# Kernel tuning notes

Measured on AMD Instinct MI355X. Metric: run time of the kernel, lower is better.

Reference implementation:

```python
import jax, jax.numpy as jnp
import numpy as np

B, H, W, C = 16, 64, 64, 256
WS = 8          # window_size
SHIFT = 4       # shift_size
HEADS = 8
HEAD_DIM = C // HEADS
N = WS * WS     # tokens per window
HID = 4 * C     # mlp hidden
EPS = 1e-5


def _rel_pos_index():
    coords = np.stack(np.meshgrid(np.arange(WS), np.arange(WS), indexing='ij'))  # [2,WS,WS]
    flat = coords.reshape(2, -1)                                                  # [2,N]
    rel = (flat[:, :, None] - flat[:, None, :]).transpose(1, 2, 0)                # [N,N,2]
    rel[:, :, 0] += WS - 1
    rel[:, :, 1] += WS - 1
    rel[:, :, 0] *= 2 * WS - 1
    return rel.sum(-1).astype(np.int32)                                           # [N,N]


def _attn_mask():
    # shifted-window region ids, identical to get_img_mask (shift == WS//2)
    img = np.zeros((H, W), dtype=np.float32)
    cnt = 0
    for hs in (slice(0, H - WS), slice(H - WS, H - SHIFT), slice(H - SHIFT, H)):
        for ws_ in (slice(0, W - WS), slice(W - WS, W - SHIFT), slice(W - SHIFT, W)):
            img[hs, ws_] = cnt
            cnt += 1
    mw = img.reshape(H // WS, WS, W // WS, WS).transpose(0, 2, 1, 3).reshape(-1, N)  # [nW,N]
    diff = mw[:, None, :] - mw[:, :, None]
    return np.where(diff != 0, -100.0, 0.0).astype(np.float32)                        # [nW,N,N]


def window_partition(x):
    # [B,H,W,C] -> [B*nW, N, C]
    x = x.reshape(B, H // WS, WS, W // WS, WS, C)
    return x.transpose(0, 1, 3, 2, 4, 5).reshape(-1, N, C)


def window_reverse(w):
    # [B*nW, WS, WS, C] -> [B,H,W,C]
    x = w.reshape(B, H // WS, W // WS, WS, WS, C)
    return x.transpose(0, 1, 3, 2, 4, 5).reshape(B, H, W, C)


def layernorm(x, g, b):
    mu = jnp.mean(x, -1, keepdims=True)
    var = jnp.mean(jnp.square(x - mu), -1, keepdims=True)
    return (x - mu) * jax.lax.rsqrt(var + EPS) * g + b


def setup_inputs() -> dict:
    key = jax.random.key(0)
    ks = jax.random.split(key, 12)
    s = 0.02
    return {
        'x': jax.random.normal(ks[0], (B, H, W, C), jnp.float32),
        'ln1_g': jnp.ones((C,), jnp.float32),
        'ln1_b': jnp.zeros((C,), jnp.float32),
        'qkv_w': jax.random.normal(ks[1], (C, 3 * C), jnp.float32) * s,
        'qkv_b': jnp.zeros((3 * C,), jnp.float32),
        'proj_w': jax.random.normal(ks[2], (C, C), jnp.float32) * s,
        'proj_b': jnp.zeros((C,), jnp.float32),
        'rel_bias_table': jax.random.normal(ks[3], ((2 * WS - 1) ** 2, HEADS), jnp.float32) * s,
        'ln2_g': jnp.ones((C,), jnp.float32),
        'ln2_b': jnp.zeros((C,), jnp.float32),
        'mlp_w1': jax.random.normal(ks[4], (C, HID), jnp.float32) * s,
        'mlp_b1': jnp.zeros((HID,), jnp.float32),
        'mlp_w2': jax.random.normal(ks[5], (HID, C), jnp.float32) * s,
        'mlp_b2': jnp.zeros((C,), jnp.float32),
        'rel_index': jnp.asarray(_rel_pos_index()),  # [N,N] int32, constant
    }


def reference(x, ln1_g, ln1_b, qkv_w, qkv_b, proj_w, proj_b, rel_bias_table,
              ln2_g, ln2_b, mlp_w1, mlp_b1, mlp_w2, mlp_b2, rel_index):
    attn_mask = jnp.asarray(_attn_mask())                 # [nW,N,N]
    nW = attn_mask.shape[0]

    shortcut = x.reshape(B, H * W, C)
    h = layernorm(shortcut, ln1_g, ln1_b).reshape(B, H, W, C)

    # cyclic shift + window partition
    h = jnp.roll(h, shift=(-SHIFT, -SHIFT), axis=(1, 2))
    xw = window_partition(h)                              # [B*nW, N, C]

    # window attention with relative position bias
    qkv = xw @ qkv_w + qkv_b                              # [B*nW, N, 3C]
    qkv = qkv.reshape(-1, N, 3, HEADS, HEAD_DIM).transpose(2, 0, 3, 1, 4)
    q, k, v = qkv[0], qkv[1], qkv[2]                      # [B*nW, heads, N, hd]
    attn = jnp.einsum('whnd,whmd->whnm', q * (HEAD_DIM ** -0.5), k)
    bias = rel_bias_table[rel_index]                      # [N,N,heads]
    attn = attn + bias.transpose(2, 0, 1)[None]           # [B*nW,heads,N,N]
    attn = attn.reshape(B, nW, HEADS, N, N) + attn_mask[None, :, None]
    attn = jax.nn.softmax(attn.reshape(-1, HEADS, N, N), axis=-1)
    out = jnp.einsum('whnm,whmd->whnd', attn, v)
    out = out.transpose(0, 2, 1, 3).reshape(-1, N, C)
    out = out @ proj_w + proj_b                           # [B*nW, N, C]

    # window reverse + reverse shift
    out = window_reverse(out.reshape(-1, WS, WS, C))
    out = jnp.roll(out, shift=(SHIFT, SHIFT), axis=(1, 2)).reshape(B, H * W, C)

    h = shortcut + out
    m = layernorm(h, ln2_g, ln2_b)
    m = jax.nn.gelu(m @ mlp_w1 + mlp_b1) @ mlp_w2 + mlp_b2
    h = h + m
    return h.reshape(B, H, W, C)
```

## Files before the change

kernel.cpp:

```cpp
#include <hip/hip_runtime.h>


typedef __attribute__((ext_vector_type(8))) short bf16x8;
typedef __attribute__((ext_vector_type(4))) float f32x4;
typedef __attribute__((ext_vector_type(16))) float f32x16;

__device__ __forceinline__ float bf2f(unsigned short h) {
    union { unsigned int u; float f; } c; c.u = ((unsigned int)h) << 16; return c.f;
}
__device__ __forceinline__ unsigned short f2bf(float f) {
    union { float f; unsigned int u; } c; c.f = f;
    unsigned int u = c.u;
    return (unsigned short)((u + 0x7FFFu + ((u >> 16) & 1u)) >> 16);
}
__device__ __forceinline__ unsigned int cvtpk_bf16(float lo, float hi) {
    unsigned int r;
    asm volatile("v_cvt_pk_bf16_f32 %0, %1, %2" : "=v"(r) : "v"(lo), "v"(hi));
    return r;
}
__device__ __forceinline__ void perm32swap(unsigned int& a, unsigned int& b) {
    asm volatile("v_permlane32_swap_b32 %0, %1" : "+v"(a), "+v"(b));
}
__device__ __forceinline__ int remap_row(int row) {
    int b  = row >> 12;
    int w6 = (row >> 6) & 63;
    int n  = row & 63;
    int hp = (((w6 >> 3) << 3) + (n >> 3) + 4) & 63;
    int wp = (((w6 & 7) << 3) + (n & 7) + 4) & 63;
    return (b << 12) | (hp << 6) | wp;
}
__device__ __forceinline__ float gelu_f(float v) {
    float u = 1.5957691216057308f * (v + 0.044715f * v * v * v);
    return v / (1.0f + __expf(-u));
}
__device__ __forceinline__ void gload16(const unsigned short* g, unsigned short* l) {
    __builtin_amdgcn_global_load_lds(
        (const __attribute__((address_space(1))) void*)g,
        (__attribute__((address_space(3))) void*)l, 16, 0, 0);
}

__global__ __launch_bounds__(256) void ln_kernel(
    const float* __restrict__ in, const float* __restrict__ g,
    const float* __restrict__ b, unsigned short* __restrict__ out, int remap)
{
    int wave = threadIdx.x >> 6, lane = threadIdx.x & 63;
    int row = (blockIdx.x << 2) + wave;
    int src = remap ? remap_row(row) : row;
    float4 xv = *(const float4*)(in + (size_t)src * 256 + (lane << 2));
    float s  = xv.x + xv.y + xv.z + xv.w;
    float ss = xv.x*xv.x + xv.y*xv.y + xv.z*xv.z + xv.w*xv.w;
#pragma unroll
    for (int off = 32; off; off >>= 1) {
        s  += __shfl_xor(s,  off, 64);
        ss += __shfl_xor(ss, off, 64);
    }
    float mu  = s * (1.0f / 256.0f);
    float inv = rsqrtf(ss * (1.0f / 256.0f) - mu * mu + 1e-5f);
    float4 gv = *(const float4*)(g + (lane << 2));
    float4 bv = *(const float4*)(b + (lane << 2));
    ushort4 o;
    o.x = f2bf((xv.x - mu) * inv * gv.x + bv.x);
    o.y = f2bf((xv.y - mu) * inv * gv.y + bv.y);
    o.z = f2bf((xv.z - mu) * inv * gv.z + bv.z);
    o.w = f2bf((xv.w - mu) * inv * gv.w + bv.w);
    *(ushort4*)(out + (size_t)row * 256 + (lane << 2)) = o;
}

__global__ __launch_bounds__(256) void bias_expand_kernel(
    const float* __restrict__ table, const int* __restrict__ relidx,
    float* __restrict__ out)
{
    int i = blockIdx.x * 256 + threadIdx.x;
    int head = i >> 12;
    int q = (i >> 6) & 63;
    int k = i & 63;
    out[i] = table[relidx[q * 64 + k] * 8 + head];
}

__global__ __launch_bounds__(256) void convert_T_kernel(
    const float* __restrict__ in, unsigned short* __restrict__ out, int K, int N)
{
    __shared__ float t[32][33];
    int kb = K >> 5;
    int bk = (blockIdx.x % kb) << 5;
    int bn = (blockIdx.x / kb) << 5;
    int r = threadIdx.x >> 5, c = threadIdx.x & 31;
#pragma unroll
    for (int i = 0; i < 4; ++i)
        t[r + i * 8][c] = in[(size_t)(bk + r + i * 8) * N + bn + c];
    __syncthreads();
#pragma unroll
    for (int i = 0; i < 4; ++i)
        out[(size_t)(bn + r + i * 8) * K + bk + c] = f2bf(t[c][r + i * 8]);
}

template<int OUT_BF16, int DO_GELU, int RESID, int QSCALE>
__global__ __launch_bounds__(256) void mgemm_kernel(
    const unsigned short* __restrict__ A, const unsigned short* __restrict__ BT,
    const float* __restrict__ bias, void* __restrict__ outp,
    const float* __restrict__ resid, int M, int N, int K)
{
    __shared__ unsigned short As[2][128 * 32];
    __shared__ unsigned short Bs[2][128 * 32];

    const int cpx = (int)gridDim.x >> 3;
    const int bid = ((int)blockIdx.x & 7) * cpx + ((int)blockIdx.x >> 3);

    const int nb = N >> 7;
    const int m0 = (bid / nb) << 7;
    const int n0 = (bid % nb) << 7;
    const int tid  = threadIdx.x;
    const int wid  = tid >> 6;
    const int lane = tid & 63;
    const int wm = (wid >> 1) << 6;
    const int wn = (wid & 1) << 6;

    const unsigned short* Ag = A  + (size_t)m0 * K;
    const unsigned short* Bg = BT + (size_t)n0 * K;
    const int s0 = tid, s1 = tid + 256;
    const size_t ra0 = (size_t)(s0 >> 2) * K + ((s0 & 3) << 3);
    const size_t ra1 = (size_t)(s1 >> 2) * K + ((s1 & 3) << 3);

    f32x4 acc[4][4] = {};
    const int fr = lane & 15;
    const int fk = (lane >> 4) << 3;

    gload16(Ag + ra0, As[0] + s0 * 8);
    gload16(Ag + ra1, As[0] + s1 * 8);
    gload16(Bg + ra0, Bs[0] + s0 * 8);
    gload16(Bg + ra1, Bs[0] + s1 * 8);
    __syncthreads();

    int cur = 0;
    for (int k0 = 0; k0 < K; k0 += 32) {
        if (k0 + 32 < K) {
            const int nxt = cur ^ 1;
            gload16(Ag + ra0 + k0 + 32, As[nxt] + s0 * 8);
            gload16(Ag + ra1 + k0 + 32, As[nxt] + s1 * 8);
            gload16(Bg + ra0 + k0 + 32, Bs[nxt] + s0 * 8);
            gload16(Bg + ra1 + k0 + 32, Bs[nxt] + s1 * 8);
        }

        bf16x8 af[4], bfr[4];
#pragma unroll
        for (int i = 0; i < 4; ++i)
            af[i] = *(const bf16x8*)(As[cur] + (wm + i * 16 + fr) * 32 + fk);
#pragma unroll
        for (int j = 0; j < 4; ++j)
            bfr[j] = *(const bf16x8*)(Bs[cur] + (wn + j * 16 + fr) * 32 + fk);
#pragma unroll
        for (int i = 0; i < 4; ++i)
#pragma unroll
            for (int j = 0; j < 4; ++j)
                acc[i][j] = __builtin_amdgcn_mfma_f32_16x16x32_bf16(
                    af[i], bfr[j], acc[i][j], 0, 0, 0);
        __syncthreads();
        cur ^= 1;
    }

#pragma unroll
    for (int i = 0; i < 4; ++i) {
#pragma unroll
        for (int j = 0; j < 4; ++j) {
            const int col = n0 + wn + j * 16 + (lane & 15);
            const float bv = bias[col];
#pragma unroll
            for (int v = 0; v < 4; ++v) {
                const int row = m0 + wm + i * 16 + ((lane >> 4) << 2) + v;
                float val = acc[i][j][v] + bv;
                if (QSCALE) { if (col < 256) val *= 0.17677669529663687f; }
                if (DO_GELU) val = gelu_f(val);
                if (OUT_BF16) {
                    ((unsigned short*)outp)[(size_t)row * N + col] = f2bf(val);
                } else {
                    const int orow = (RESID == 2) ? remap_row(row) : row;
                    const float r = RESID ? resid[(size_t)orow * N + col] : 0.0f;
                    ((float*)outp)[(size_t)orow * N + col] = r + val;
                }
            }
        }
    }
}

__global__ __launch_bounds__(64, 3) void attn_kernel(
    const unsigned short* __restrict__ qkv,
    const float* __restrict__ bexp,
    unsigned short* __restrict__ out)
{
    __shared__ unsigned short VT[2048];
    const int bid  = blockIdx.x;
    const int widx = bid & 1023;
    const int head = bid >> 10;
    const int l  = threadIdx.x;
    const int lo = l & 31, hi = l >> 5;

    const unsigned short* base = qkv + (size_t)widx * 64 * 768;

#pragma unroll
    for (int c = 0; c < 4; ++c) {
        union { bf16x8 v; unsigned short s[8]; } u;
        u.v = *(const bf16x8*)(base + (size_t)l * 768 + 512 + head * 32 + c * 8);
#pragma unroll
        for (int e = 0; e < 8; ++e) {
            int d = c * 8 + e;
            int wb = ((d * 64 + l) * 2) ^ ((d & 7) << 4);
            *(unsigned short*)((char*)VT + wb) = u.s[e];
        }
    }

    f32x16 acc[2][2] = {};
#pragma unroll
    for (int kd = 0; kd < 2; ++kd) {
        const int coff = head * 32 + kd * 16 + hi * 8;
        bf16x8 kf0 = *(const bf16x8*)(base + (size_t)lo        * 768 + 256 + coff);
        bf16x8 kf1 = *(const bf16x8*)(base + (size_t)(32 + lo) * 768 + 256 + coff);
        bf16x8 qf0 = *(const bf16x8*)(base + (size_t)lo        * 768 + coff);
        bf16x8 qf1 = *(const bf16x8*)(base + (size_t)(32 + lo) * 768 + coff);
        acc[0][0] = __builtin_amdgcn_mfma_f32_32x32x16_bf16(kf0, qf0, acc[0][0], 0, 0, 0);
        acc[0][1] = __builtin_amdgcn_mfma_f32_32x32x16_bf16(kf0, qf1, acc[0][1], 0, 0, 0);
        acc[1][0] = __builtin_amdgcn_mfma_f32_32x32x16_bf16(kf1, qf0, acc[1][0], 0, 0, 0);
        acc[1][1] = __builtin_amdgcn_mfma_f32_32x32x16_bf16(kf1, qf1, acc[1][1], 0, 0, 0);
    }

#pragma unroll
    for (int qb = 0; qb < 2; ++qb) {
        const float* bq = bexp + head * 4096 + (qb * 32 + lo) * 64;
#pragma unroll
        for (int kb = 0; kb < 2; ++kb)
#pragma unroll
            for (int j = 0; j < 4; ++j) {
                float4 b4 = *(const float4*)(bq + kb * 32 + j * 8 + hi * 4);
                acc[kb][qb][4 * j + 0] += b4.x;
                acc[kb][qb][4 * j + 1] += b4.y;
                acc[kb][qb][4 * j + 2] += b4.z;
                acc[kb][qb][4 * j + 3] += b4.w;
            }
    }

    const int w6 = widx & 63;
    if (((w6 >> 3) == 7) || ((w6 & 7) == 7)) {
#pragma unroll
        for (int qb = 0; qb < 2; ++qb) {
            int nq = qb * 32 + lo;
            int phq = ((w6 >> 3) << 3) + (nq >> 3), pwq = ((w6 & 7) << 3) + (nq & 7);
            int rq = ((phq < 56) ? 0 : ((phq < 60) ? 1 : 2)) * 3
                   + ((pwq < 56) ? 0 : ((pwq < 60) ? 1 : 2));
#pragma unroll
            for (int kb = 0; kb < 2; ++kb)
#pragma unroll
                for (int r = 0; r < 16; ++r) {
                    int nk = kb * 32 + (r & 3) + 8 * (r >> 2) + 4 * hi;
                    int phk = ((w6 >> 3) << 3) + (nk >> 3), pwk = ((w6 & 7) << 3) + (nk & 7);
                    int rk = ((phk < 56) ? 0 : ((phk < 60) ? 1 : 2)) * 3
                           + ((pwk < 56) ? 0 : ((pwk < 60) ? 1 : 2));
                    if (rk != rq) acc[kb][qb][r] -= 100.0f;
                }
        }
    }

#pragma unroll
    for (int qb = 0; qb < 2; ++qb) {
        float mx = acc[0][qb][0];
#pragma unroll
        for (int r = 1; r < 16; ++r) mx = fmaxf(mx, acc[0][qb][r]);
#pragma unroll
        for (int r = 0; r < 16; ++r) mx = fmaxf(mx, acc[1][qb][r]);
        mx = fmaxf(mx, __shfl_xor(mx, 32, 64));
        float sum = 0.f;
#pragma unroll
        for (int kb = 0; kb < 2; ++kb)
#pragma unroll
            for (int r = 0; r < 16; ++r) {
                float e = __expf(acc[kb][qb][r] - mx);
                acc[kb][qb][r] = e;
                sum += e;
            }
        sum += __shfl_xor(sum, 32, 64);
        float inv = 1.0f / sum;
#pragma unroll
        for (int kb = 0; kb < 2; ++kb)
#pragma unroll
            for (int r = 0; r < 16; ++r) acc[kb][qb][r] *= inv;
    }

    f32x16 o[2] = {};
#pragma unroll
    for (int ks = 0; ks < 4; ++ks) {
        const int s8 = (ks & 1) * 8, kb = ks >> 1;
        const int rb = ((lo * 64 + 16 * ks + 8 * hi) * 2) ^ ((lo & 7) << 4);
        bf16x8 vb = *(const bf16x8*)((const char*)VT + rb);
#pragma unroll
        for (int qb = 0; qb < 2; ++qb) {
            unsigned int a0 = cvtpk_bf16(acc[kb][qb][s8 + 0], acc[kb][qb][s8 + 1]);
            unsigned int b0 = cvtpk_bf16(acc[kb][qb][s8 + 4], acc[kb][qb][s8 + 5]);
            unsigned int a1 = cvtpk_bf16(acc[kb][qb][s8 + 2], acc[kb][qb][s8 + 3]);
            unsigned int b1 = cvtpk_bf16(acc[kb][qb][s8 + 6], acc[kb][qb][s8 + 7]);
            perm32swap(a0, b0);
            perm32swap(a1, b1);
            union { unsigned int u[4]; bf16x8 v; } w;
            w.u[0] = a0; w.u[1] = a1; w.u[2] = b0; w.u[3] = b1;
            o[qb] = __builtin_amdgcn_mfma_f32_32x32x16_bf16(w.v, vb, o[qb], 0, 0, 0);
        }
    }

    unsigned short* ob = out + (size_t)widx * 64 * 256 + head * 32 + lo;
#pragma unroll
    for (int qb = 0; qb < 2; ++qb)
#pragma unroll
        for (int r = 0; r < 16; ++r) {
            int q = qb * 32 + (r & 3) + 8 * (r >> 2) + 4 * hi;
            ob[(size_t)q * 256] = f2bf(o[qb][r]);
        }
}

extern "C" void kernel_launch(void* const* d_in, const int* in_sizes, int n_in,
                              void* d_out, int out_size, void* d_ws, size_t ws_size,
                              hipStream_t stream)
{
    const float* x      = (const float*)d_in[0];
    const float* ln1_g  = (const float*)d_in[1];
    const float* ln1_b  = (const float*)d_in[2];
    const float* qkv_w  = (const float*)d_in[3];
    const float* qkv_b  = (const float*)d_in[4];
    const float* proj_w = (const float*)d_in[5];
    const float* proj_b = (const float*)d_in[6];
    const float* table  = (const float*)d_in[7];
    const float* ln2_g  = (const float*)d_in[8];
    const float* ln2_b  = (const float*)d_in[9];
    const float* w1     = (const float*)d_in[10];
    const float* b1     = (const float*)d_in[11];
    const float* w2     = (const float*)d_in[12];
    const float* b2     = (const float*)d_in[13];
    const int*   relidx = (const int*)d_in[14];
    float* out = (float*)d_out;

    char* w = (char*)d_ws;
    unsigned short* xw   = (unsigned short*)w;
    unsigned short* qkvb = (unsigned short*)(w + (32u << 20));
    float*          h2   = (float*)(w + (160u << 20));
    float*          bexp = (float*)(w + (224u << 20));
    unsigned short* qkvT = (unsigned short*)(w + (224u << 20) + (128u << 10));
    unsigned short* prjT = qkvT + 768 * 256;
    unsigned short* w1T  = prjT + 256 * 256;
    unsigned short* w2T  = w1T + 1024 * 256;

    convert_T_kernel<<<192, 256, 0, stream>>>(qkv_w, qkvT, 256, 768);
    convert_T_kernel<<< 64, 256, 0, stream>>>(proj_w, prjT, 256, 256);
    convert_T_kernel<<<256, 256, 0, stream>>>(w1, w1T, 256, 1024);
    convert_T_kernel<<<256, 256, 0, stream>>>(w2, w2T, 1024, 256);
    ln_kernel<<<16384, 256, 0, stream>>>(x, ln1_g, ln1_b, xw, 1);
    bias_expand_kernel<<<128, 256, 0, stream>>>(table, relidx, bexp);
    mgemm_kernel<1, 0, 0, 1><<<512 * 6, 256, 0, stream>>>(xw, qkvT, qkv_b, (void*)qkvb,
                                                          nullptr, 65536, 768, 256);
    attn_kernel<<<8192, 64, 0, stream>>>(qkvb, bexp, xw);
    mgemm_kernel<0, 0, 2, 0><<<512 * 2, 256, 0, stream>>>(xw, prjT, proj_b, (void*)h2,
                                                          x, 65536, 256, 256);
    ln_kernel<<<16384, 256, 0, stream>>>(h2, ln2_g, ln2_b, xw, 0);
    mgemm_kernel<1, 1, 0, 0><<<512 * 8, 256, 0, stream>>>(xw, w1T, b1, (void*)qkvb,
                                                          nullptr, 65536, 1024, 256);
    mgemm_kernel<0, 0, 1, 0><<<512 * 2, 256, 0, stream>>>(qkvb, w2T, b2, (void*)out,
                                                          h2, 65536, 256, 1024);
}
```

Before: 323.5 us.

## Fuse MLP fc1+GELU+fc2 into one kernel and swizzle GEMM LDS layout

Replaces the two MLP GEMM launches with a single fused kernel. Each block keeps a 64-row activation tile in LDS, computes 128-column hidden chunks with GELU into LDS, and accumulates the second GEMM in registers, so the 65536x1024 bf16 hidden tensor never goes to HBM. The generic GEMM also gets an XOR swizzle on its LDS tiles to cut bank conflicts. In exchange, the fused kernel runs only 1024 blocks with heavy LDS use (about 80KB), which lowers occupancy and adds many barriers per chunk.

```diff
diff --git a/kernel.cpp b/kernel.cpp
--- a/kernel.cpp
+++ b/kernel.cpp
@@ -118,12 +118,13 @@
     const unsigned short* Ag = A  + (size_t)m0 * K;
     const unsigned short* Bg = BT + (size_t)n0 * K;
     const int s0 = tid, s1 = tid + 256;
-    const size_t ra0 = (size_t)(s0 >> 2) * K + ((s0 & 3) << 3);
-    const size_t ra1 = (size_t)(s1 >> 2) * K + ((s1 & 3) << 3);
+    const size_t ra0 = (size_t)(s0 >> 2) * K + (((s0 & 3) ^ ((s0 >> 2) & 3)) << 3);
+    const size_t ra1 = (size_t)(s1 >> 2) * K + (((s1 & 3) ^ ((s1 >> 2) & 3)) << 3);
 
     f32x4 acc[4][4] = {};
     const int fr = lane & 15;
-    const int fk = (lane >> 4) << 3;
+    const int fq = lane >> 4;
+    const int axor = ((fq ^ (fr & 3)) << 3);
 
     gload16(Ag + ra0, As[0] + s0 * 8);
     gload16(Ag + ra1, As[0] + s1 * 8);
@@ -144,10 +145,10 @@
         bf16x8 af[4], bfr[4];
 #pragma unroll
         for (int i = 0; i < 4; ++i)
-            af[i] = *(const bf16x8*)(As[cur] + (wm + i * 16 + fr) * 32 + fk);
+            af[i] = *(const bf16x8*)(As[cur] + (wm + i * 16 + fr) * 32 + axor);
 #pragma unroll
         for (int j = 0; j < 4; ++j)
-            bfr[j] = *(const bf16x8*)(Bs[cur] + (wn + j * 16 + fr) * 32 + fk);
+            bfr[j] = *(const bf16x8*)(Bs[cur] + (wn + j * 16 + fr) * 32 + axor);
 #pragma unroll
         for (int i = 0; i < 4; ++i)
 #pragma unroll
@@ -180,6 +181,155 @@
             }
         }
     }
+}
+
+__global__ __launch_bounds__(256) void mlp_fused_kernel(
+    const unsigned short* __restrict__ A,
+    const unsigned short* __restrict__ W1T,
+    const float* __restrict__ b1v,
+    const unsigned short* __restrict__ W2T,
+    const float* __restrict__ b2v,
+    const float* __restrict__ h2,
+    float* __restrict__ outp)
+{
+    __shared__ unsigned short Al[64 * 256];
+    __shared__ unsigned short Hl[64 * 128];
+    __shared__ unsigned short Bsh[2][8192];
+
+    const int m0 = (int)blockIdx.x << 6;
+    const int tid = threadIdx.x;
+    const int lane = tid & 63;
+    const int wid = tid >> 6;
+    const int fr = lane & 15, fq = lane >> 4;
+    const int wn1 = wid << 5;
+    const int wn2 = wid << 6;
+
+#pragma unroll
+    for (int i = 0; i < 8; ++i) {
+        int s = tid + (i << 8);
+        int row = s >> 5;
+        int ce = ((s & 31) ^ (row & 7)) << 3;
+        gload16(A + (size_t)(m0 + row) * 256 + ce, Al + s * 8);
+    }
+
+#define STAGE_B1(c, t, buf)                                                   \
+    {                                                                         \
+        _Pragma("unroll")                                                     \
+        for (int i_ = 0; i_ < 4; ++i_) {                                      \
+            int s_ = tid + (i_ << 8);                                         \
+            int r_ = s_ >> 3;                                                 \
+            int ce_ = ((s_ & 7) ^ (r_ & 7)) << 3;                             \
+            gload16(W1T + (size_t)((c) * 128 + r_) * 256 + (t) * 64 + ce_,    \
+                    Bsh[buf] + s_ * 8);                                       \
+        }                                                                     \
+    }
+#define STAGE_B2(c, t, buf)                                                   \
+    {                                                                         \
+        _Pragma("unroll")                                                     \
+        for (int i_ = 0; i_ < 4; ++i_) {                                      \
+            int s_ = tid + (i_ << 8);                                         \
+            int r_ = s_ >> 2;                                                 \
+            int ce_ = ((s_ & 3) ^ (r_ & 3)) << 3;                             \
+            gload16(W2T + (size_t)r_ * 1024 + (c) * 128 + (t) * 32 + ce_,     \
+                    Bsh[buf] + s_ * 8);                                       \
+        }                                                                     \
+    }
+
+    f32x4 acc2[4][4] = {};
+    STAGE_B1(0, 0, 0);
+    __syncthreads();
+
+    for (int c = 0; c < 8; ++c) {
+        f32x4 acc1[4][2] = {};
+#pragma unroll
+        for (int t = 0; t < 4; ++t) {
+            if (t < 3) { STAGE_B1(c, t + 1, (t + 1) & 1); }
+            else       { STAGE_B2(c, 0, 0); }
+            bf16x8 a[4][2], b[2][2];
+#pragma unroll
+            for (int i = 0; i < 4; ++i) {
+                int row = i * 16 + fr;
+#pragma unroll
+                for (int kk = 0; kk < 2; ++kk)
+                    a[i][kk] = *(const bf16x8*)(Al + row * 256 +
+                        ((t * 64 + kk * 32 + fq * 8) ^ ((row & 7) << 3)));
+            }
+#pragma unroll
+            for (int j = 0; j < 2; ++j) {
+                int row = wn1 + j * 16 + fr;
+#pragma unroll
+                for (int kk = 0; kk < 2; ++kk)
+                    b[j][kk] = *(const bf16x8*)(Bsh[t & 1] + row * 64 +
+                        ((kk * 32 + fq * 8) ^ ((row & 7) << 3)));
+            }
+#pragma unroll
+            for (int i = 0; i < 4; ++i)
+#pragma unroll
+                for (int j = 0; j < 2; ++j)
+#pragma unroll
+                    for (int kk = 0; kk < 2; ++kk)
+                        acc1[i][j] = __builtin_amdgcn_mfma_f32_16x16x32_bf16(
+                            a[i][kk], b[j][kk], acc1[i][j], 0, 0, 0);
+            __syncthreads();
+        }
+#pragma unroll
+        for (int j = 0; j < 2; ++j) {
+            int col = wn1 + j * 16 + fr;
+            float bv = b1v[c * 128 + col];
+#pragma unroll
+            for (int i = 0; i < 4; ++i)
+#pragma unroll
+                for (int v = 0; v < 4; ++v) {
+                    int row = i * 16 + fq * 4 + v;
+                    float val = gelu_f(acc1[i][j][v] + bv);
+                    int lin = (row << 8) + (col << 1);
+                    lin ^= (row & 7) << 4;
+                    *(unsigned short*)((char*)Hl + lin) = f2bf(val);
+                }
+        }
+        __syncthreads();
+#pragma unroll
+        for (int t = 0; t < 4; ++t) {
+            if (t < 3)      { STAGE_B2(c, t + 1, (t + 1) & 1); }
+            else if (c < 7) { STAGE_B1(c + 1, 0, 0); }
+            bf16x8 ha[4], bb[4];
+#pragma unroll
+            for (int i = 0; i < 4; ++i) {
+                int row = i * 16 + fr;
+                ha[i] = *(const bf16x8*)(Hl + row * 128 +
+                    ((t * 32 + fq * 8) ^ ((row & 7) << 3)));
+            }
+#pragma unroll
+            for (int j = 0; j < 4; ++j) {
+                int row = wn2 + j * 16 + fr;
+                bb[j] = *(const bf16x8*)(Bsh[t & 1] + row * 32 +
+                    ((fq * 8) ^ ((row & 3) << 3)));
+            }
+#pragma unroll
+            for (int i = 0; i < 4; ++i)
+#pragma unroll
+                for (int j = 0; j < 4; ++j)
+                    acc2[i][j] = __builtin_amdgcn_mfma_f32_16x16x32_bf16(
+                        ha[i], bb[j], acc2[i][j], 0, 0, 0);
+            __syncthreads();
+        }
+    }
+#undef STAGE_B1
+#undef STAGE_B2
+
+#pragma unroll
+    for (int i = 0; i < 4; ++i)
+#pragma unroll
+        for (int j = 0; j < 4; ++j) {
+            const int col = wn2 + j * 16 + fr;
+            const float bv = b2v[col];
+#pragma unroll
+            for (int v = 0; v < 4; ++v) {
+                const int row = m0 + i * 16 + fq * 4 + v;
+                const size_t off = (size_t)row * 256 + col;
+                outp[off] = acc2[i][j][v] + bv + h2[off];
+            }
+        }
 }
 
 __global__ __launch_bounds__(64, 3) void attn_kernel(
@@ -356,8 +506,5 @@
     mgemm_kernel<0, 0, 2, 0><<<512 * 2, 256, 0, stream>>>(xw, prjT, proj_b, (void*)h2,
                                                           x, 65536, 256, 256);
     ln_kernel<<<16384, 256, 0, stream>>>(h2, ln2_g, ln2_b, xw, 0);
-    mgemm_kernel<1, 1, 0, 0><<<512 * 8, 256, 0, stream>>>(xw, w1T, b1, (void*)qkvb,
-                                                          nullptr, 65536, 1024, 256);
-    mgemm_kernel<0, 0, 1, 0><<<512 * 2, 256, 0, stream>>>(qkvb, w2T, b2, (void*)out,
-                                                          h2, 65536, 256, 1024);
-}
+    mlp_fused_kernel<<<1024, 256, 0, stream>>>(xw, w1T, b1, w2T, b2, h2, out);
+}
```

After: 392.3 us. 1.21x slower.

## Swizzle GEMM LDS tiles, swap MFMA operands for vectorized epilogue, merge prep kernels

Applied to the files above, without the earlier changes.

The GEMM's LDS tile layout gets an XOR swizzle on the k-chunk index, so fragment reads hit fewer bank conflicts. MFMA operands are swapped so each lane holds four consecutive output columns. That lets the epilogue do float4 bias and residual loads and packed bf16 or float4 stores instead of scalar strided writes. The four weight-transpose launches and the bias-expand launch are merged into one prep kernel to cut launch overhead.

```diff
diff --git a/kernel.cpp b/kernel.cpp
--- a/kernel.cpp
+++ b/kernel.cpp
@@ -66,25 +66,14 @@
     *(ushort4*)(out + (size_t)row * 256 + (lane << 2)) = o;
 }
 
-__global__ __launch_bounds__(256) void bias_expand_kernel(
-    const float* __restrict__ table, const int* __restrict__ relidx,
-    float* __restrict__ out)
-{
-    int i = blockIdx.x * 256 + threadIdx.x;
-    int head = i >> 12;
-    int q = (i >> 6) & 63;
-    int k = i & 63;
-    out[i] = table[relidx[q * 64 + k] * 8 + head];
-}
-
-__global__ __launch_bounds__(256) void convert_T_kernel(
-    const float* __restrict__ in, unsigned short* __restrict__ out, int K, int N)
-{
-    __shared__ float t[32][33];
+__device__ __forceinline__ void convT_body(
+    const float* __restrict__ in, unsigned short* __restrict__ out,
+    int K, int N, int b, float (*t)[33], int tid)
+{
     int kb = K >> 5;
-    int bk = (blockIdx.x % kb) << 5;
-    int bn = (blockIdx.x / kb) << 5;
-    int r = threadIdx.x >> 5, c = threadIdx.x & 31;
+    int bk = (b % kb) << 5;
+    int bn = (b / kb) << 5;
+    int r = tid >> 5, c = tid & 31;
 #pragma unroll
     for (int i = 0; i < 4; ++i)
         t[r + i * 8][c] = in[(size_t)(bk + r + i * 8) * N + bn + c];
@@ -92,6 +81,29 @@
 #pragma unroll
     for (int i = 0; i < 4; ++i)
         out[(size_t)(bn + r + i * 8) * K + bk + c] = f2bf(t[c][r + i * 8]);
+}
+
+__global__ __launch_bounds__(256) void prep_kernel(
+    const float* __restrict__ qkv_w, const float* __restrict__ proj_w,
+    const float* __restrict__ w1, const float* __restrict__ w2,
+    unsigned short* __restrict__ qkvT, unsigned short* __restrict__ prjT,
+    unsigned short* __restrict__ w1T, unsigned short* __restrict__ w2T,
+    const float* __restrict__ table, const int* __restrict__ relidx,
+    float* __restrict__ bexp)
+{
+    __shared__ float t[32][33];
+    const int b = blockIdx.x, tid = threadIdx.x;
+    if      (b < 192) convT_body(qkv_w, qkvT, 256,  768, b,       t, tid);
+    else if (b < 256) convT_body(proj_w, prjT, 256,  256, b - 192, t, tid);
+    else if (b < 512) convT_body(w1,    w1T,  256, 1024, b - 256, t, tid);
+    else if (b < 768) convT_body(w2,    w2T, 1024,  256, b - 512, t, tid);
+    else {
+        int i = (b - 768) * 256 + tid;
+        int head = i >> 12;
+        int q = (i >> 6) & 63;
+        int k = i & 63;
+        bexp[i] = table[relidx[q * 64 + k] * 8 + head];
+    }
 }
 
 template<int OUT_BF16, int DO_GELU, int RESID, int QSCALE>
@@ -118,12 +130,13 @@
     const unsigned short* Ag = A  + (size_t)m0 * K;
     const unsigned short* Bg = BT + (size_t)n0 * K;
     const int s0 = tid, s1 = tid + 256;
-    const size_t ra0 = (size_t)(s0 >> 2) * K + ((s0 & 3) << 3);
-    const size_t ra1 = (size_t)(s1 >> 2) * K + ((s1 & 3) << 3);
+    const size_t ra0 = (size_t)(s0 >> 2) * K + (((s0 & 3) ^ ((s0 >> 2) & 3)) << 3);
+    const size_t ra1 = (size_t)(s1 >> 2) * K + (((s1 & 3) ^ ((s1 >> 2) & 3)) << 3);
 
     f32x4 acc[4][4] = {};
     const int fr = lane & 15;
-    const int fk = (lane >> 4) << 3;
+    const int fq = lane >> 4;
+    const int axor = ((fq ^ (fr & 3)) << 3);
 
     gload16(Ag + ra0, As[0] + s0 * 8);
     gload16(Ag + ra1, As[0] + s1 * 8);
@@ -144,39 +157,54 @@
         bf16x8 af[4], bfr[4];
 #pragma unroll
         for (int i = 0; i < 4; ++i)
-            af[i] = *(const bf16x8*)(As[cur] + (wm + i * 16 + fr) * 32 + fk);
+            af[i] = *(const bf16x8*)(As[cur] + (wm + i * 16 + fr) * 32 + axor);
 #pragma unroll
         for (int j = 0; j < 4; ++j)
-            bfr[j] = *(const bf16x8*)(Bs[cur] + (wn + j * 16 + fr) * 32 + fk);
-#pragma unroll
-        for (int i = 0; i < 4; ++i)
-#pragma unroll
-            for (int j = 0; j < 4; ++j)
-                acc[i][j] = __builtin_amdgcn_mfma_f32_16x16x32_bf16(
-                    af[i], bfr[j], acc[i][j], 0, 0, 0);
+            bfr[j] = *(const bf16x8*)(Bs[cur] + (wn + j * 16 + fr) * 32 + axor);
+#pragma unroll
+        for (int j = 0; j < 4; ++j)
+#pragma unroll
+            for (int i = 0; i < 4; ++i)
+                acc[j][i] = __builtin_amdgcn_mfma_f32_16x16x32_bf16(
+                    bfr[j], af[i], acc[j][i], 0, 0, 0);
         __syncthreads();
         cur ^= 1;
     }
 
 #pragma unroll
-    for (int i = 0; i < 4; ++i) {
-#pragma unroll
-        for (int j = 0; j < 4; ++j) {
-            const int col = n0 + wn + j * 16 + (lane & 15);
-            const float bv = bias[col];
-#pragma unroll
-            for (int v = 0; v < 4; ++v) {
-                const int row = m0 + wm + i * 16 + ((lane >> 4) << 2) + v;
-                float val = acc[i][j][v] + bv;
-                if (QSCALE) { if (col < 256) val *= 0.17677669529663687f; }
-                if (DO_GELU) val = gelu_f(val);
-                if (OUT_BF16) {
-                    ((unsigned short*)outp)[(size_t)row * N + col] = f2bf(val);
+    for (int j = 0; j < 4; ++j) {
+        const int colbase = n0 + wn + j * 16 + (fq << 2);
+        const float4 b4 = *(const float4*)(bias + colbase);
+#pragma unroll
+        for (int i = 0; i < 4; ++i) {
+            const int row = m0 + wm + i * 16 + fr;
+            float v0 = acc[j][i][0] + b4.x;
+            float v1 = acc[j][i][1] + b4.y;
+            float v2 = acc[j][i][2] + b4.z;
+            float v3 = acc[j][i][3] + b4.w;
+            if (QSCALE && colbase < 256) {
+                v0 *= 0.17677669529663687f; v1 *= 0.17677669529663687f;
+                v2 *= 0.17677669529663687f; v3 *= 0.17677669529663687f;
+            }
+            if (DO_GELU) {
+                v0 = gelu_f(v0); v1 = gelu_f(v1); v2 = gelu_f(v2); v3 = gelu_f(v3);
+            }
+            if (OUT_BF16) {
+                uint2 pp;
+                pp.x = cvtpk_bf16(v0, v1);
+                pp.y = cvtpk_bf16(v2, v3);
+                *(uint2*)((unsigned short*)outp + (size_t)row * N + colbase) = pp;
+            } else {
+                const int orow = (RESID == 2) ? remap_row(row) : row;
+                float4 o4;
+                if (RESID) {
+                    const float4 r4 = *(const float4*)(resid + (size_t)orow * N + colbase);
+                    o4.x = v0 + r4.x; o4.y = v1 + r4.y;
+                    o4.z = v2 + r4.z; o4.w = v3 + r4.w;
                 } else {
-                    const int orow = (RESID == 2) ? remap_row(row) : row;
-                    const float r = RESID ? resid[(size_t)orow * N + col] : 0.0f;
-                    ((float*)outp)[(size_t)orow * N + col] = r + val;
+                    o4.x = v0; o4.y = v1; o4.z = v2; o4.w = v3;
                 }
+                *(float4*)((float*)outp + (size_t)orow * N + colbase) = o4;
             }
         }
     }
@@ -344,12 +372,10 @@
     unsigned short* w1T  = prjT + 256 * 256;
     unsigned short* w2T  = w1T + 1024 * 256;
 
-    convert_T_kernel<<<192, 256, 0, stream>>>(qkv_w, qkvT, 256, 768);
-    convert_T_kernel<<< 64, 256, 0, stream>>>(proj_w, prjT, 256, 256);
-    convert_T_kernel<<<256, 256, 0, stream>>>(w1, w1T, 256, 1024);
-    convert_T_kernel<<<256, 256, 0, stream>>>(w2, w2T, 1024, 256);
+    prep_kernel<<<896, 256, 0, stream>>>(qkv_w, proj_w, w1, w2,
+                                         qkvT, prjT, w1T, w2T,
+                                         table, relidx, bexp);
     ln_kernel<<<16384, 256, 0, stream>>>(x, ln1_g, ln1_b, xw, 1);
-    bias_expand_kernel<<<128, 256, 0, stream>>>(table, relidx, bexp);
     mgemm_kernel<1, 0, 0, 1><<<512 * 6, 256, 0, stream>>>(xw, qkvT, qkv_b, (void*)qkvb,
                                                           nullptr, 65536, 768, 256);
     attn_kernel<<<8192, 64, 0, stream>>>(qkvb, bexp, xw);
```

Result: slower. 331.4 us (+2.5%).
